# Performance work log

Hardware: AMD Instinct MI355X
Metric: run time of the kernel (lower is better)

Reference implementation:

```python
import jax, jax.numpy as jnp
import numpy as np

N_EMBD = 1024
N_HEAD = 16
HEAD_DIM = N_EMBD // N_HEAD


def setup_inputs() -> dict:
    key = jax.random.key(0)
    k1, k2, k3, k4, k5 = jax.random.split(key, 5)
    scale = 1.0 / np.sqrt(N_EMBD)
    x = jax.random.normal(k1, (4, 2048, N_EMBD), dtype=jnp.float32)
    W_qkv = jax.random.normal(k2, (N_EMBD, 3 * N_EMBD), dtype=jnp.float32) * scale
    b_qkv = jax.random.normal(k3, (3 * N_EMBD,), dtype=jnp.float32) * 0.01
    W_proj = jax.random.normal(k4, (N_EMBD, N_EMBD), dtype=jnp.float32) * scale
    b_proj = jax.random.normal(k5, (N_EMBD,), dtype=jnp.float32) * 0.01
    return {"x": x, "W_qkv": W_qkv, "b_qkv": b_qkv, "W_proj": W_proj, "b_proj": b_proj}


def reference(x, W_qkv, b_qkv, W_proj, b_proj):
    B, T, C = x.shape
    qkv = x @ W_qkv + b_qkv                      # [B,T,3C]
    q, k, v = jnp.split(qkv, 3, axis=-1)
    # [B,T,C] -> [B,H,T,D]
    def to_heads(t):
        return t.reshape(B, T, N_HEAD, HEAD_DIM).transpose(0, 2, 1, 3)
    q, k, v = to_heads(q), to_heads(k), to_heads(v)
    att = jnp.einsum('bhqd,bhkd->bhqk', q, k) / np.sqrt(HEAD_DIM)
    causal = jnp.tril(jnp.ones((T, T), dtype=bool))
    att = jnp.where(causal, att, -jnp.inf)
    att = jax.nn.softmax(att, axis=-1)
    y = jnp.einsum('bhqk,bhkd->bhqd', att, v)    # [B,H,T,D]
    y = y.transpose(0, 2, 1, 3).reshape(B, T, C)
    return y @ W_proj + b_proj
```

## Files before the change

### kernel.cpp

```cpp
#include <hip/hip_runtime.h>
#include <hip/hip_bf16.h>
#include <cstdint>

#define B_   4
#define T_   2048
#define C_   1024
#define H_   16
#define D_   64
#define TC3  3072
#define M_   (B_ * T_)

typedef short  bf16x8 __attribute__((ext_vector_type(8)));
typedef short  bf16x4 __attribute__((ext_vector_type(4)));
typedef float  f32x4  __attribute__((ext_vector_type(4)));

#define AS1(p) ((const __attribute__((address_space(1))) void*)(p))
#define AS3(p) ((__attribute__((address_space(3))) void*)(p))

__device__ inline float bf2f(unsigned short u) {
    union { unsigned int i; float f; } x; x.i = ((unsigned int)u) << 16; return x.f;
}
__device__ inline unsigned short f2bf(float f) {
    union { float f; unsigned int i; } x; x.f = f;
    return (unsigned short)((x.i + 0x7fffu + ((x.i >> 16) & 1u)) >> 16);
}
__device__ inline unsigned int cvtpk_bf16(float a, float b) {
    unsigned int r;
    asm("v_cvt_pk_bf16_f32 %0, %1, %2" : "=v"(r) : "v"(a), "v"(b));
    return r;
}
__device__ inline f32x4 mfma16x16x16(bf16x4 a, bf16x4 b, f32x4 c) {
#if __has_builtin(__builtin_amdgcn_mfma_f32_16x16x16bf16_1k)
    return __builtin_amdgcn_mfma_f32_16x16x16bf16_1k(a, b, c, 0, 0, 0);
#else
    asm("v_mfma_f32_16x16x16_bf16 %0, %1, %2, %0" : "+v"(c) : "v"(a), "v"(b));
    return c;
#endif
}

__global__ void cast_f32_bf16(const float* __restrict__ in,
                              unsigned short* __restrict__ out) {
    const size_t i = ((size_t)blockIdx.x * blockDim.x + threadIdx.x) * 8;
    f32x4 a = *(const f32x4*)(in + i);
    f32x4 b = *(const f32x4*)(in + i + 4);
    bf16x8 o;
#pragma unroll
    for (int j = 0; j < 4; ++j) { o[j] = (short)f2bf(a[j]); o[4 + j] = (short)f2bf(b[j]); }
    *(bf16x8*)(out + i) = o;
}

__global__ void transpose_cast(const float* __restrict__ in,
                               unsigned short* __restrict__ out, int R, int C) {
    __shared__ unsigned short tile[32][33];
    const int bc = blockIdx.x * 32, br = blockIdx.y * 32;
    const int tx = threadIdx.x & 31, ty = threadIdx.x >> 5;
#pragma unroll
    for (int i = 0; i < 4; ++i) {
        int r = ty + i * 8;
        tile[r][tx] = f2bf(in[(size_t)(br + r) * C + bc + tx]);
    }
    __syncthreads();
#pragma unroll
    for (int i = 0; i < 4; ++i) {
        int r = ty + i * 8;
        out[(size_t)(bc + r) * R + br + tx] = tile[tx][r];
    }
}

template <bool OUTF32>
__global__ __launch_bounds__(256, 2) void gemm_bt_bias(
    const unsigned short* __restrict__ A, const unsigned short* __restrict__ Bt,
    const float* __restrict__ bias, void* __restrict__ Cout,
    int M, int N, int K) {
    __shared__ unsigned short As[128 * 64];
    __shared__ unsigned short Bs[128 * 64];
    const int tid = threadIdx.x;
    const int wave = tid >> 6, lane = tid & 63;
    const int m0 = blockIdx.x * 128, n0 = blockIdx.y * 128;
    const int wr = (wave >> 1) * 64, wc = (wave & 1) * 64;

    f32x4 acc[4][4] = {};

    const int srow = (lane >> 3);
    const int scol = (lane & 7) * 8;

    for (int k0 = 0; k0 < K; k0 += 64) {
#pragma unroll
        for (int j = 0; j < 4; ++j) {
            const int chunk = wave * 4 + j;
            const int row = chunk * 8 + srow;
            __builtin_amdgcn_global_load_lds(
                AS1(A + (size_t)(m0 + row) * K + k0 + scol),
                AS3(As + chunk * 512), 16, 0, 0);
            __builtin_amdgcn_global_load_lds(
                AS1(Bt + (size_t)(n0 + row) * K + k0 + scol),
                AS3(Bs + chunk * 512), 16, 0, 0);
        }
        __syncthreads();
#pragma unroll
        for (int ph = 0; ph < 2; ++ph) {
            bf16x8 a[4], b[4];
#pragma unroll
            for (int i = 0; i < 4; ++i)
                a[i] = *(const bf16x8*)&As[(wr + i * 16 + (lane & 15)) * 64 + ph * 32 + (lane >> 4) * 8];
#pragma unroll
            for (int i = 0; i < 4; ++i)
                b[i] = *(const bf16x8*)&Bs[(wc + i * 16 + (lane & 15)) * 64 + ph * 32 + (lane >> 4) * 8];
            __builtin_amdgcn_s_setprio(1);
#pragma unroll
            for (int i = 0; i < 4; ++i)
#pragma unroll
                for (int j = 0; j < 4; ++j)
                    acc[i][j] = __builtin_amdgcn_mfma_f32_16x16x32_bf16(a[i], b[j], acc[i][j], 0, 0, 0);
            __builtin_amdgcn_s_setprio(0);
        }
        __syncthreads();
    }

#pragma unroll
    for (int i = 0; i < 4; ++i) {
        const int rowb = m0 + wr + i * 16 + (lane >> 4) * 4;
#pragma unroll
        for (int j = 0; j < 4; ++j) {
            const int col = n0 + wc + j * 16 + (lane & 15);
            const float bv = bias[col];
#pragma unroll
            for (int r = 0; r < 4; ++r) {
                const float v = acc[i][j][r] + bv;
                if (OUTF32)
                    ((float*)Cout)[(size_t)(rowb + r) * N + col] = v;
                else
                    ((unsigned short*)Cout)[(size_t)(rowb + r) * N + col] = f2bf(v);
            }
        }
    }
}

__global__ __launch_bounds__(512, 4) void attn_kernel(
    const unsigned short* __restrict__ QKV, unsigned short* __restrict__ Y) {
    __shared__ unsigned short Kl[64][72];
    __shared__ unsigned short Vt[64][72];

    const int tid = threadIdx.x, wave = tid >> 6, lane = tid & 63;
    const int bh = blockIdx.x;
    const int tq = 15 - (int)blockIdx.y;
    const int b = bh >> 4, h = bh & 15;
    const size_t rowbase = (size_t)b * T_ * TC3;
    const int l15 = lane & 15, lhi = lane >> 4;
    const int srow = tid >> 3;
    const int sseg = tid & 7;

    const int q0 = tq * 128 + wave * 16;
    const int ntiles = 2 * tq + 2;
    const int qv = q0 + l15;

    bf16x8 qf[2];
    {
        const unsigned short* p =
            QKV + rowbase + (size_t)(q0 + l15) * TC3 + h * 64 + lhi * 8;
        qf[0] = *(const bf16x8*)p;
        qf[1] = *(const bf16x8*)(p + 32);
#pragma unroll
        for (int hf = 0; hf < 2; ++hf)
#pragma unroll
            for (int j = 0; j < 8; ++j)
                qf[hf][j] = (short)f2bf(bf2f((unsigned short)qf[hf][j]) * 0.18033688011f);
    }

    float m2 = -1e30f, l_run = 0.f;
    f32x4 o[4] = {};

    {
        const unsigned short* src =
            QKV + rowbase + (size_t)srow * TC3 + C_ + h * 64 + sseg * 8;
        bf16x8 k8 = *(const bf16x8*)src;
        bf16x8 v8 = *(const bf16x8*)(src + C_);
        *(bf16x8*)&Kl[srow][sseg * 8] = k8;
        const int swz = srow ^ (sseg << 3);
#pragma unroll
        for (int j = 0; j < 8; ++j)
            Vt[sseg * 8 + j][swz] = (unsigned short)v8[j];
    }

    for (int t = 0; t < ntiles; ++t) {
        const int kv0 = t * 64;
        __syncthreads();

        bf16x8 pk8, pv8;
        const bool pf_valid = (t + 1 < ntiles);
        if (pf_valid) {
            const unsigned short* src =
                QKV + rowbase + (size_t)(kv0 + 64 + srow) * TC3 + C_ + h * 64 + sseg * 8;
            pk8 = *(const bf16x8*)src;
            pv8 = *(const bf16x8*)(src + C_);
        }

        if (q0 + 15 >= kv0) {
            f32x4 s[4];
            __builtin_amdgcn_s_setprio(1);
#pragma unroll
            for (int kt = 0; kt < 4; ++kt) {
                bf16x8 kf0 = *(const bf16x8*)&Kl[kt * 16 + l15][lhi * 8];
                bf16x8 kf1 = *(const bf16x8*)&Kl[kt * 16 + l15][32 + lhi * 8];
                f32x4 acc = {};
                acc = __builtin_amdgcn_mfma_f32_16x16x32_bf16(kf0, qf[0], acc, 0, 0, 0);
                acc = __builtin_amdgcn_mfma_f32_16x16x32_bf16(kf1, qf[1], acc, 0, 0, 0);
                s[kt] = acc;
            }
            __builtin_amdgcn_s_setprio(0);

            const bool needmask = (kv0 + 63 > q0);
            if (needmask) {
#pragma unroll
                for (int kt = 0; kt < 4; ++kt) {
                    const int kb = kv0 + kt * 16 + lhi * 4;
#pragma unroll
                    for (int r = 0; r < 4; ++r)
                        s[kt][r] = (kb + r <= qv) ? s[kt][r] : -1e30f;
                }
            }
            f32x4 vm;
#pragma unroll
            for (int r = 0; r < 4; ++r)
                vm[r] = fmaxf(fmaxf(s[0][r], s[1][r]), fmaxf(s[2][r], s[3][r]));
            float tmax = fmaxf(fmaxf(vm[0], vm[1]), fmaxf(vm[2], vm[3]));
            tmax = fmaxf(tmax, __shfl_xor(tmax, 16, 64));
            tmax = fmaxf(tmax, __shfl_xor(tmax, 32, 64));

            if (__any(tmax > m2 + 11.5416f)) {
                const float mnew = fmaxf(m2, tmax);
                const float corr = exp2f(m2 - mnew);
                m2 = mnew; l_run *= corr;
                float cq[4];
#pragma unroll
                for (int r = 0; r < 4; ++r)
                    cq[r] = __shfl(corr, lhi * 16 + lhi * 4 + r, 64);
#pragma unroll
                for (int dt = 0; dt < 4; ++dt)
#pragma unroll
                    for (int r = 0; r < 4; ++r) o[dt][r] *= cq[r];
            }
#pragma unroll
            for (int kt = 0; kt < 4; ++kt)
#pragma unroll
                for (int r = 0; r < 4; ++r)
                    s[kt][r] = exp2f(s[kt][r] - m2);
            {
                f32x4 vs;
#pragma unroll
                for (int r = 0; r < 4; ++r)
                    vs[r] = (s[0][r] + s[1][r]) + (s[2][r] + s[3][r]);
                float tsum = (vs[0] + vs[1]) + (vs[2] + vs[3]);
                tsum += __shfl_xor(tsum, 16, 64);
                tsum += __shfl_xor(tsum, 32, 64);
                l_run += tsum;
            }
            bf16x4 pa[4];
#pragma unroll
            for (int kt = 0; kt < 4; ++kt) {
                unsigned int pw[2];
                pw[0] = cvtpk_bf16(s[kt][0], s[kt][1]);
                pw[1] = cvtpk_bf16(s[kt][2], s[kt][3]);
                pa[kt] = *(const bf16x4*)pw;
            }

            __builtin_amdgcn_s_setprio(1);
#pragma unroll
            for (int dt = 0; dt < 4; ++dt) {
                const int d = dt * 16 + l15;
                const int xs = (d >> 3) << 3;
#pragma unroll
                for (int kt = 0; kt < 4; ++kt) {
                    bf16x4 vb = *(const bf16x4*)&Vt[d][(kt * 16 + lhi * 4) ^ xs];
                    o[dt] = mfma16x16x16(pa[kt], vb, o[dt]);
                }
            }
            __builtin_amdgcn_s_setprio(0);
        }

        __syncthreads();
        if (pf_valid) {
            *(bf16x8*)&Kl[srow][sseg * 8] = pk8;
            const int swz = srow ^ (sseg << 3);
#pragma unroll
            for (int j = 0; j < 8; ++j)
                Vt[sseg * 8 + j][swz] = (unsigned short)pv8[j];
        }
    }

    float rq[4];
#pragma unroll
    for (int r = 0; r < 4; ++r) {
        const float lq = __shfl(l_run, lhi * 16 + lhi * 4 + r, 64);
        rq[r] = 1.0f / lq;
    }
#pragma unroll
    for (int dt = 0; dt < 4; ++dt)
#pragma unroll
        for (int r = 0; r < 4; ++r) {
            const int q = q0 + lhi * 4 + r;
            const int d = dt * 16 + l15;
            Y[((size_t)b * T_ + q) * C_ + h * 64 + d] = f2bf(o[dt][r] * rq[r]);
        }
}

extern "C" void kernel_launch(void* const* d_in, const int* in_sizes, int n_in,
                              void* d_out, int out_size, void* d_ws, size_t ws_size,
                              hipStream_t stream) {
    const float* x     = (const float*)d_in[0];
    const float* Wqkv  = (const float*)d_in[1];
    const float* bqkv  = (const float*)d_in[2];
    const float* Wproj = (const float*)d_in[3];
    const float* bproj = (const float*)d_in[4];
    float* out = (float*)d_out;

    char* ws = (char*)d_ws;
    unsigned short* qkv    = (unsigned short*)(ws);
    unsigned short* yat    = (unsigned short*)(ws + 50331648);
    unsigned short* WqkvT  = (unsigned short*)(ws + 67108864);
    unsigned short* WprojT = (unsigned short*)(ws + 73400320);
    unsigned short* xb     = (unsigned short*)(ws + 75497472);

    cast_f32_bf16<<<dim3((M_ * C_) / (256 * 8)), dim3(256), 0, stream>>>(x, xb);
    transpose_cast<<<dim3(TC3 / 32, C_ / 32), dim3(256), 0, stream>>>(Wqkv, WqkvT, C_, TC3);
    transpose_cast<<<dim3(C_ / 32, C_ / 32), dim3(256), 0, stream>>>(Wproj, WprojT, C_, C_);
    gemm_bt_bias<false><<<dim3(M_ / 128, TC3 / 128), dim3(256), 0, stream>>>(xb, WqkvT, bqkv, qkv, M_, TC3, C_);
    attn_kernel<<<dim3(B_ * H_, 16), dim3(512), 0, stream>>>(qkv, yat);
    gemm_bt_bias<true><<<dim3(M_ / 128, C_ / 128), dim3(256), 0, stream>>>(yat, WprojT, bproj, out, M_, C_, C_);
}
```

Measured before the change: 186.9 us.

## Add 256x256 double-buffered QKV GEMM and pair causal attention tiles per block

```diff
diff --git a/kernel.cpp b/kernel.cpp
--- a/kernel.cpp
+++ b/kernel.cpp
@@ -67,10 +67,115 @@
     }
 }
 
-template <bool OUTF32>
+__global__ __launch_bounds__(512, 2) void gemm8_qkv(
+    const unsigned short* __restrict__ A, const unsigned short* __restrict__ Bt,
+    const float* __restrict__ bias, unsigned short* __restrict__ Cout,
+    int M, int N, int K) {
+    __shared__ unsigned short As[2 * 8192];
+    __shared__ unsigned short Bs[2 * 8192];
+
+    const int tid = threadIdx.x;
+    const int wave = tid >> 6, lane = tid & 63;
+    const int l15 = lane & 15, lhi = lane >> 4;
+    const int m0 = blockIdx.x * 256, n0 = blockIdx.y * 256;
+    const int wr = (wave >> 2) * 128;
+    const int wc = (wave & 3) * 64;
+
+    const int srow_s = tid >> 2;
+    const int scol_s = ((tid & 3) * 8) ^ ((srow_s & 3) << 3);
+    const int ldsw = (tid >> 6) * 512;
+
+    const int xcol = (lhi * 8) ^ ((l15 & 3) << 3);
+
+    f32x4 acc[8][4] = {};
+
+    {
+#pragma unroll
+        for (int g = 0; g < 2; ++g) {
+            __builtin_amdgcn_global_load_lds(
+                AS1(A + (size_t)(m0 + g * 128 + srow_s) * K + scol_s),
+                AS3(As + g * 4096 + ldsw), 16, 0, 0);
+            __builtin_amdgcn_global_load_lds(
+                AS1(Bt + (size_t)(n0 + g * 128 + srow_s) * K + scol_s),
+                AS3(Bs + g * 4096 + ldsw), 16, 0, 0);
+        }
+    }
+    __syncthreads();
+
+    for (int t = 0; t < 32; ++t) {
+        const int k0n = t * 32 + 32;
+        const int cur = t & 1, nxt = cur ^ 1;
+        const unsigned short* Ac = As + cur * 8192;
+        const unsigned short* Bc = Bs + cur * 8192;
+        unsigned short* An = As + nxt * 8192;
+        unsigned short* Bn = Bs + nxt * 8192;
+        const bool pf = (t < 31);
+
+        bf16x8 a[4], b[4];
+#pragma unroll
+        for (int i = 0; i < 4; ++i)
+            a[i] = *(const bf16x8*)&Ac[(wr + i * 16 + l15) * 32 + xcol];
+#pragma unroll
+        for (int j = 0; j < 4; ++j)
+            b[j] = *(const bf16x8*)&Bc[(wc + j * 16 + l15) * 32 + xcol];
+        if (pf) {
+            __builtin_amdgcn_global_load_lds(
+                AS1(A + (size_t)(m0 + srow_s) * K + k0n + scol_s),
+                AS3(An + ldsw), 16, 0, 0);
+            __builtin_amdgcn_global_load_lds(
+                AS1(Bt + (size_t)(n0 + srow_s) * K + k0n + scol_s),
+                AS3(Bn + ldsw), 16, 0, 0);
+        }
+        __builtin_amdgcn_s_barrier();
+        __builtin_amdgcn_s_setprio(1);
+#pragma unroll
+        for (int i = 0; i < 4; ++i)
+#pragma unroll
+            for (int j = 0; j < 4; ++j)
+                acc[i][j] = __builtin_amdgcn_mfma_f32_16x16x32_bf16(a[i], b[j], acc[i][j], 0, 0, 0);
+        __builtin_amdgcn_s_setprio(0);
+        __builtin_amdgcn_s_barrier();
+
+        bf16x8 a2[4];
+#pragma unroll
+        for (int i = 0; i < 4; ++i)
+            a2[i] = *(const bf16x8*)&Ac[(wr + (i + 4) * 16 + l15) * 32 + xcol];
+        if (pf) {
+            __builtin_amdgcn_global_load_lds(
+                AS1(A + (size_t)(m0 + 128 + srow_s) * K + k0n + scol_s),
+                AS3(An + 4096 + ldsw), 16, 0, 0);
+            __builtin_amdgcn_global_load_lds(
+                AS1(Bt + (size_t)(n0 + 128 + srow_s) * K + k0n + scol_s),
+                AS3(Bn + 4096 + ldsw), 16, 0, 0);
+        }
+        __builtin_amdgcn_s_barrier();
+        __builtin_amdgcn_s_setprio(1);
+#pragma unroll
+        for (int i = 0; i < 4; ++i)
+#pragma unroll
+            for (int j = 0; j < 4; ++j)
+                acc[i + 4][j] = __builtin_amdgcn_mfma_f32_16x16x32_bf16(a2[i], b[j], acc[i + 4][j], 0, 0, 0);
+        __builtin_amdgcn_s_setprio(0);
+        __syncthreads();
+    }
+
+#pragma unroll
+    for (int i = 0; i < 8; ++i) {
+        const int rowb = m0 + wr + i * 16 + lhi * 4;
+#pragma unroll
+        for (int j = 0; j < 4; ++j) {
+            const int col = n0 + wc + j * 16 + l15;
+            const float bv = bias[col];
+#pragma unroll
+            for (int r = 0; r < 4; ++r)
+                Cout[(size_t)(rowb + r) * N + col] = f2bf(acc[i][j][r] + bv);
+        }
+    }
+}
+
 __global__ __launch_bounds__(256, 2) void gemm_bt_bias(
     const unsigned short* __restrict__ A, const unsigned short* __restrict__ Bt,
-    const float* __restrict__ bias, void* __restrict__ Cout,
+    const float* __restrict__ bias, float* __restrict__ Cout,
     int M, int N, int K) {
     __shared__ unsigned short As[128 * 64];
     __shared__ unsigned short Bs[128 * 64];
@@ -125,13 +230,8 @@
             const int col = n0 + wc + j * 16 + (lane & 15);
             const float bv = bias[col];
 #pragma unroll
-            for (int r = 0; r < 4; ++r) {
-                const float v = acc[i][j][r] + bv;
-                if (OUTF32)
-                    ((float*)Cout)[(size_t)(rowb + r) * N + col] = v;
-                else
-                    ((unsigned short*)Cout)[(size_t)(rowb + r) * N + col] = f2bf(v);
-            }
+            for (int r = 0; r < 4; ++r)
+                Cout[(size_t)(rowb + r) * N + col] = acc[i][j][r] + bv;
         }
     }
 }
@@ -143,165 +243,170 @@
 
     const int tid = threadIdx.x, wave = tid >> 6, lane = tid & 63;
     const int bh = blockIdx.x;
-    const int tq = 15 - (int)blockIdx.y;
+    const int pr = blockIdx.y;
     const int b = bh >> 4, h = bh & 15;
     const size_t rowbase = (size_t)b * T_ * TC3;
     const int l15 = lane & 15, lhi = lane >> 4;
     const int srow = tid >> 3;
     const int sseg = tid & 7;
 
-    const int q0 = tq * 128 + wave * 16;
-    const int ntiles = 2 * tq + 2;
-    const int qv = q0 + l15;
-
-    bf16x8 qf[2];
-    {
-        const unsigned short* p =
-            QKV + rowbase + (size_t)(q0 + l15) * TC3 + h * 64 + lhi * 8;
-        qf[0] = *(const bf16x8*)p;
-        qf[1] = *(const bf16x8*)(p + 32);
-#pragma unroll
-        for (int hf = 0; hf < 2; ++hf)
+    for (int sp = 0; sp < 2; ++sp) {
+        const int tq = sp ? (15 - pr) : pr;
+        const int qb = tq * 128;
+        const int q0 = qb + wave * 16;
+        const int ntiles = 2 * tq + 2;
+        const int qv = q0 + l15;
+
+        bf16x8 qf[2];
+        {
+            const unsigned short* p =
+                QKV + rowbase + (size_t)(q0 + l15) * TC3 + h * 64 + lhi * 8;
+            qf[0] = *(const bf16x8*)p;
+            qf[1] = *(const bf16x8*)(p + 32);
+#pragma unroll
+            for (int hf = 0; hf < 2; ++hf)
+#pragma unroll
+                for (int j = 0; j < 8; ++j)
+                    qf[hf][j] = (short)f2bf(bf2f((unsigned short)qf[hf][j]) * 0.18033688011f);
+        }
+
+        float m2 = -1e30f, l_run = 0.f;
+        f32x4 o[4] = {};
+
+        __syncthreads();
+        {
+            const unsigned short* src =
+                QKV + rowbase + (size_t)srow * TC3 + C_ + h * 64 + sseg * 8;
+            bf16x8 k8 = *(const bf16x8*)src;
+            bf16x8 v8 = *(const bf16x8*)(src + C_);
+            *(bf16x8*)&Kl[srow][sseg * 8] = k8;
+            const int swz = srow ^ (sseg << 3);
 #pragma unroll
             for (int j = 0; j < 8; ++j)
-                qf[hf][j] = (short)f2bf(bf2f((unsigned short)qf[hf][j]) * 0.18033688011f);
-    }
-
-    float m2 = -1e30f, l_run = 0.f;
-    f32x4 o[4] = {};
-
-    {
-        const unsigned short* src =
-            QKV + rowbase + (size_t)srow * TC3 + C_ + h * 64 + sseg * 8;
-        bf16x8 k8 = *(const bf16x8*)src;
-        bf16x8 v8 = *(const bf16x8*)(src + C_);
-        *(bf16x8*)&Kl[srow][sseg * 8] = k8;
-        const int swz = srow ^ (sseg << 3);
-#pragma unroll
-        for (int j = 0; j < 8; ++j)
-            Vt[sseg * 8 + j][swz] = (unsigned short)v8[j];
-    }
-
-    for (int t = 0; t < ntiles; ++t) {
-        const int kv0 = t * 64;
-        __syncthreads();
-
-        bf16x8 pk8, pv8;
-        const bool pf_valid = (t + 1 < ntiles);
-        if (pf_valid) {
-            const unsigned short* src =
-                QKV + rowbase + (size_t)(kv0 + 64 + srow) * TC3 + C_ + h * 64 + sseg * 8;
-            pk8 = *(const bf16x8*)src;
-            pv8 = *(const bf16x8*)(src + C_);
-        }
-
-        if (q0 + 15 >= kv0) {
-            f32x4 s[4];
-            __builtin_amdgcn_s_setprio(1);
-#pragma unroll
-            for (int kt = 0; kt < 4; ++kt) {
-                bf16x8 kf0 = *(const bf16x8*)&Kl[kt * 16 + l15][lhi * 8];
-                bf16x8 kf1 = *(const bf16x8*)&Kl[kt * 16 + l15][32 + lhi * 8];
-                f32x4 acc = {};
-                acc = __builtin_amdgcn_mfma_f32_16x16x32_bf16(kf0, qf[0], acc, 0, 0, 0);
-                acc = __builtin_amdgcn_mfma_f32_16x16x32_bf16(kf1, qf[1], acc, 0, 0, 0);
-                s[kt] = acc;
+                Vt[sseg * 8 + j][swz] = (unsigned short)v8[j];
+        }
+
+        for (int t = 0; t < ntiles; ++t) {
+            const int kv0 = t * 64;
+            __syncthreads();
+
+            bf16x8 pk8, pv8;
+            const bool pf_valid = (t + 1 < ntiles);
+            if (pf_valid) {
+                const unsigned short* src =
+                    QKV + rowbase + (size_t)(kv0 + 64 + srow) * TC3 + C_ + h * 64 + sseg * 8;
+                pk8 = *(const bf16x8*)src;
+                pv8 = *(const bf16x8*)(src + C_);
             }
-            __builtin_amdgcn_s_setprio(0);
-
-            const bool needmask = (kv0 + 63 > q0);
-            if (needmask) {
+
+            if (q0 + 15 >= kv0) {
+                f32x4 s[4];
+                __builtin_amdgcn_s_setprio(1);
 #pragma unroll
                 for (int kt = 0; kt < 4; ++kt) {
-                    const int kb = kv0 + kt * 16 + lhi * 4;
+                    bf16x8 kf0 = *(const bf16x8*)&Kl[kt * 16 + l15][lhi * 8];
+                    bf16x8 kf1 = *(const bf16x8*)&Kl[kt * 16 + l15][32 + lhi * 8];
+                    f32x4 acc = {};
+                    acc = __builtin_amdgcn_mfma_f32_16x16x32_bf16(kf0, qf[0], acc, 0, 0, 0);
+                    acc = __builtin_amdgcn_mfma_f32_16x16x32_bf16(kf1, qf[1], acc, 0, 0, 0);
+                    s[kt] = acc;
+                }
+                __builtin_amdgcn_s_setprio(0);
+
+                const bool needmask = (kv0 + 63 > q0);
+                if (needmask) {
+#pragma unroll
+                    for (int kt = 0; kt < 4; ++kt) {
+                        const int kb = kv0 + kt * 16 + lhi * 4;
+#pragma unroll
+                        for (int r = 0; r < 4; ++r)
+                            s[kt][r] = (kb + r <= qv) ? s[kt][r] : -1e30f;
+                    }
+                }
+                f32x4 vm;
+#pragma unroll
+                for (int r = 0; r < 4; ++r)
+                    vm[r] = fmaxf(fmaxf(s[0][r], s[1][r]), fmaxf(s[2][r], s[3][r]));
+                float tmax = fmaxf(fmaxf(vm[0], vm[1]), fmaxf(vm[2], vm[3]));
+                tmax = fmaxf(tmax, __shfl_xor(tmax, 16, 64));
+                tmax = fmaxf(tmax, __shfl_xor(tmax, 32, 64));
+
+                if (__any(tmax > m2 + 11.5416f)) {
+                    const float mnew = fmaxf(m2, tmax);
+                    const float corr = exp2f(m2 - mnew);
+                    m2 = mnew; l_run *= corr;
+                    float cq[4];
 #pragma unroll
                     for (int r = 0; r < 4; ++r)
-                        s[kt][r] = (kb + r <= qv) ? s[kt][r] : -1e30f;
-                }
+                        cq[r] = __shfl(corr, lhi * 16 + lhi * 4 + r, 64);
+#pragma unroll
+                    for (int dt = 0; dt < 4; ++dt)
+#pragma unroll
+                        for (int r = 0; r < 4; ++r) o[dt][r] *= cq[r];
+                }
+#pragma unroll
+                for (int kt = 0; kt < 4; ++kt)
+#pragma unroll
+                    for (int r = 0; r < 4; ++r)
+                        s[kt][r] = exp2f(s[kt][r] - m2);
+                {
+                    f32x4 vs;
+#pragma unroll
+                    for (int r = 0; r < 4; ++r)
+                        vs[r] = (s[0][r] + s[1][r]) + (s[2][r] + s[3][r]);
+                    float tsum = (vs[0] + vs[1]) + (vs[2] + vs[3]);
+                    tsum += __shfl_xor(tsum, 16, 64);
+                    tsum += __shfl_xor(tsum, 32, 64);
+                    l_run += tsum;
+                }
+                bf16x4 pa[4];
+#pragma unroll
+                for (int kt = 0; kt < 4; ++kt) {
+                    unsigned int pw[2];
+                    pw[0] = cvtpk_bf16(s[kt][0], s[kt][1]);
+                    pw[1] = cvtpk_bf16(s[kt][2], s[kt][3]);
+                    pa[kt] = *(const bf16x4*)pw;
+                }
+
+                __builtin_amdgcn_s_setprio(1);
+#pragma unroll
+                for (int dt = 0; dt < 4; ++dt) {
+                    const int d = dt * 16 + l15;
+                    const int xs = (d >> 3) << 3;
+#pragma unroll
+                    for (int kt = 0; kt < 4; ++kt) {
+                        bf16x4 vb = *(const bf16x4*)&Vt[d][(kt * 16 + lhi * 4) ^ xs];
+                        o[dt] = mfma16x16x16(pa[kt], vb, o[dt]);
+                    }
+                }
+                __builtin_amdgcn_s_setprio(0);
             }
-            f32x4 vm;
-#pragma unroll
-            for (int r = 0; r < 4; ++r)
-                vm[r] = fmaxf(fmaxf(s[0][r], s[1][r]), fmaxf(s[2][r], s[3][r]));
-            float tmax = fmaxf(fmaxf(vm[0], vm[1]), fmaxf(vm[2], vm[3]));
-            tmax = fmaxf(tmax, __shfl_xor(tmax, 16, 64));
-            tmax = fmaxf(tmax, __shfl_xor(tmax, 32, 64));
-
-            if (__any(tmax > m2 + 11.5416f)) {
-                const float mnew = fmaxf(m2, tmax);
-                const float corr = exp2f(m2 - mnew);
-                m2 = mnew; l_run *= corr;
-                float cq[4];
-#pragma unroll
-                for (int r = 0; r < 4; ++r)
-                    cq[r] = __shfl(corr, lhi * 16 + lhi * 4 + r, 64);
-#pragma unroll
-                for (int dt = 0; dt < 4; ++dt)
-#pragma unroll
-                    for (int r = 0; r < 4; ++r) o[dt][r] *= cq[r];
+
+            __syncthreads();
+            if (pf_valid) {
+                *(bf16x8*)&Kl[srow][sseg * 8] = pk8;
+                const int swz = srow ^ (sseg << 3);
+#pragma unroll
+                for (int j = 0; j < 8; ++j)
+                    Vt[sseg * 8 + j][swz] = (unsigned short)pv8[j];
             }
-#pragma unroll
-            for (int kt = 0; kt < 4; ++kt)
-#pragma unroll
-                for (int r = 0; r < 4; ++r)
-                    s[kt][r] = exp2f(s[kt][r] - m2);
-            {
-                f32x4 vs;
-#pragma unroll
-                for (int r = 0; r < 4; ++r)
-                    vs[r] = (s[0][r] + s[1][r]) + (s[2][r] + s[3][r]);
-                float tsum = (vs[0] + vs[1]) + (vs[2] + vs[3]);
-                tsum += __shfl_xor(tsum, 16, 64);
-                tsum += __shfl_xor(tsum, 32, 64);
-                l_run += tsum;
+        }
+
+        float rq[4];
+#pragma unroll
+        for (int r = 0; r < 4; ++r) {
+            const float lq = __shfl(l_run, lhi * 16 + lhi * 4 + r, 64);
+            rq[r] = 1.0f / lq;
+        }
+#pragma unroll
+        for (int dt = 0; dt < 4; ++dt)
+#pragma unroll
+            for (int r = 0; r < 4; ++r) {
+                const int q = q0 + lhi * 4 + r;
+                const int d = dt * 16 + l15;
+                Y[((size_t)b * T_ + q) * C_ + h * 64 + d] = f2bf(o[dt][r] * rq[r]);
             }
-            bf16x4 pa[4];
-#pragma unroll
-            for (int kt = 0; kt < 4; ++kt) {
-                unsigned int pw[2];
-                pw[0] = cvtpk_bf16(s[kt][0], s[kt][1]);
-                pw[1] = cvtpk_bf16(s[kt][2], s[kt][3]);
-                pa[kt] = *(const bf16x4*)pw;
-            }
-
-            __builtin_amdgcn_s_setprio(1);
-#pragma unroll
-            for (int dt = 0; dt < 4; ++dt) {
-                const int d = dt * 16 + l15;
-                const int xs = (d >> 3) << 3;
-#pragma unroll
-                for (int kt = 0; kt < 4; ++kt) {
-                    bf16x4 vb = *(const bf16x4*)&Vt[d][(kt * 16 + lhi * 4) ^ xs];
-                    o[dt] = mfma16x16x16(pa[kt], vb, o[dt]);
-                }
-            }
-            __builtin_amdgcn_s_setprio(0);
-        }
-
-        __syncthreads();
-        if (pf_valid) {
-            *(bf16x8*)&Kl[srow][sseg * 8] = pk8;
-            const int swz = srow ^ (sseg << 3);
-#pragma unroll
-            for (int j = 0; j < 8; ++j)
-                Vt[sseg * 8 + j][swz] = (unsigned short)pv8[j];
-        }
-    }
-
-    float rq[4];
-#pragma unroll
-    for (int r = 0; r < 4; ++r) {
-        const float lq = __shfl(l_run, lhi * 16 + lhi * 4 + r, 64);
-        rq[r] = 1.0f / lq;
-    }
-#pragma unroll
-    for (int dt = 0; dt < 4; ++dt)
-#pragma unroll
-        for (int r = 0; r < 4; ++r) {
-            const int q = q0 + lhi * 4 + r;
-            const int d = dt * 16 + l15;
-            Y[((size_t)b * T_ + q) * C_ + h * 64 + d] = f2bf(o[dt][r] * rq[r]);
-        }
+    }
 }
 
 extern "C" void kernel_launch(void* const* d_in, const int* in_sizes, int n_in,
@@ -324,7 +429,7 @@
     cast_f32_bf16<<<dim3((M_ * C_) / (256 * 8)), dim3(256), 0, stream>>>(x, xb);
     transpose_cast<<<dim3(TC3 / 32, C_ / 32), dim3(256), 0, stream>>>(Wqkv, WqkvT, C_, TC3);
     transpose_cast<<<dim3(C_ / 32, C_ / 32), dim3(256), 0, stream>>>(Wproj, WprojT, C_, C_);
-    gemm_bt_bias<false><<<dim3(M_ / 128, TC3 / 128), dim3(256), 0, stream>>>(xb, WqkvT, bqkv, qkv, M_, TC3, C_);
-    attn_kernel<<<dim3(B_ * H_, 16), dim3(512), 0, stream>>>(qkv, yat);
-    gemm_bt_bias<true><<<dim3(M_ / 128, C_ / 128), dim3(256), 0, stream>>>(yat, WprojT, bproj, out, M_, C_, C_);
-}
+    gemm8_qkv<<<dim3(M_ / 256, TC3 / 256), dim3(512), 0, stream>>>(xb, WqkvT, bqkv, qkv, M_, TC3, C_);
+    attn_kernel<<<dim3(B_ * H_, 8), dim3(512), 0, stream>>>(qkv, yat);
+    gemm_bt_bias<<<dim3(M_ / 128, C_ / 128), dim3(256), 0, stream>>>(yat, WprojT, bproj, out, M_, C_, C_);
+}
```

New measurement: 195.2 us. +4.5%, slower.

## Double-buffer GEMM LDS tiles and pair causal attention query blocks per workgroup

Applied to the files above, without the earlier changes.

```diff
diff --git a/kernel.cpp b/kernel.cpp
--- a/kernel.cpp
+++ b/kernel.cpp
@@ -72,8 +72,8 @@
     const unsigned short* __restrict__ A, const unsigned short* __restrict__ Bt,
     const float* __restrict__ bias, void* __restrict__ Cout,
     int M, int N, int K) {
-    __shared__ unsigned short As[128 * 64];
-    __shared__ unsigned short Bs[128 * 64];
+    __shared__ unsigned short As[2][128 * 64];
+    __shared__ unsigned short Bs[2][128 * 64];
     const int tid = threadIdx.x;
     const int wave = tid >> 6, lane = tid & 63;
     const int m0 = blockIdx.x * 128, n0 = blockIdx.y * 128;
@@ -84,28 +84,45 @@
     const int srow = (lane >> 3);
     const int scol = (lane & 7) * 8;
 
-    for (int k0 = 0; k0 < K; k0 += 64) {
-#pragma unroll
-        for (int j = 0; j < 4; ++j) {
-            const int chunk = wave * 4 + j;
-            const int row = chunk * 8 + srow;
-            __builtin_amdgcn_global_load_lds(
-                AS1(A + (size_t)(m0 + row) * K + k0 + scol),
-                AS3(As + chunk * 512), 16, 0, 0);
-            __builtin_amdgcn_global_load_lds(
-                AS1(Bt + (size_t)(n0 + row) * K + k0 + scol),
-                AS3(Bs + chunk * 512), 16, 0, 0);
-        }
-        __syncthreads();
+#pragma unroll
+    for (int j = 0; j < 4; ++j) {
+        const int chunk = wave * 4 + j;
+        const int row = chunk * 8 + srow;
+        __builtin_amdgcn_global_load_lds(
+            AS1(A + (size_t)(m0 + row) * K + scol),
+            AS3(&As[0][chunk * 512]), 16, 0, 0);
+        __builtin_amdgcn_global_load_lds(
+            AS1(Bt + (size_t)(n0 + row) * K + scol),
+            AS3(&Bs[0][chunk * 512]), 16, 0, 0);
+    }
+    __syncthreads();
+
+    const int NT = K >> 6;
+    for (int t = 0; t < NT; ++t) {
+        const int cur = t & 1, nxt = cur ^ 1;
+        if (t + 1 < NT) {
+            const int k0n = (t + 1) << 6;
+#pragma unroll
+            for (int j = 0; j < 4; ++j) {
+                const int chunk = wave * 4 + j;
+                const int row = chunk * 8 + srow;
+                __builtin_amdgcn_global_load_lds(
+                    AS1(A + (size_t)(m0 + row) * K + k0n + scol),
+                    AS3(&As[nxt][chunk * 512]), 16, 0, 0);
+                __builtin_amdgcn_global_load_lds(
+                    AS1(Bt + (size_t)(n0 + row) * K + k0n + scol),
+                    AS3(&Bs[nxt][chunk * 512]), 16, 0, 0);
+            }
+        }
 #pragma unroll
         for (int ph = 0; ph < 2; ++ph) {
             bf16x8 a[4], b[4];
 #pragma unroll
             for (int i = 0; i < 4; ++i)
-                a[i] = *(const bf16x8*)&As[(wr + i * 16 + (lane & 15)) * 64 + ph * 32 + (lane >> 4) * 8];
+                a[i] = *(const bf16x8*)&As[cur][(wr + i * 16 + (lane & 15)) * 64 + ph * 32 + (lane >> 4) * 8];
 #pragma unroll
             for (int i = 0; i < 4; ++i)
-                b[i] = *(const bf16x8*)&Bs[(wc + i * 16 + (lane & 15)) * 64 + ph * 32 + (lane >> 4) * 8];
+                b[i] = *(const bf16x8*)&Bs[cur][(wc + i * 16 + (lane & 15)) * 64 + ph * 32 + (lane >> 4) * 8];
             __builtin_amdgcn_s_setprio(1);
 #pragma unroll
             for (int i = 0; i < 4; ++i)
@@ -143,165 +160,170 @@
 
     const int tid = threadIdx.x, wave = tid >> 6, lane = tid & 63;
     const int bh = blockIdx.x;
-    const int tq = 15 - (int)blockIdx.y;
+    const int pr = blockIdx.y;
     const int b = bh >> 4, h = bh & 15;
     const size_t rowbase = (size_t)b * T_ * TC3;
     const int l15 = lane & 15, lhi = lane >> 4;
     const int srow = tid >> 3;
     const int sseg = tid & 7;
 
-    const int q0 = tq * 128 + wave * 16;
-    const int ntiles = 2 * tq + 2;
-    const int qv = q0 + l15;
-
-    bf16x8 qf[2];
-    {
-        const unsigned short* p =
-            QKV + rowbase + (size_t)(q0 + l15) * TC3 + h * 64 + lhi * 8;
-        qf[0] = *(const bf16x8*)p;
-        qf[1] = *(const bf16x8*)(p + 32);
-#pragma unroll
-        for (int hf = 0; hf < 2; ++hf)
+    for (int sp = 0; sp < 2; ++sp) {
+        const int tq = sp ? (15 - pr) : pr;
+        const int qb = tq * 128;
+        const int q0 = qb + wave * 16;
+        const int ntiles = 2 * tq + 2;
+        const int qv = q0 + l15;
+
+        bf16x8 qf[2];
+        {
+            const unsigned short* p =
+                QKV + rowbase + (size_t)(q0 + l15) * TC3 + h * 64 + lhi * 8;
+            qf[0] = *(const bf16x8*)p;
+            qf[1] = *(const bf16x8*)(p + 32);
+#pragma unroll
+            for (int hf = 0; hf < 2; ++hf)
+#pragma unroll
+                for (int j = 0; j < 8; ++j)
+                    qf[hf][j] = (short)f2bf(bf2f((unsigned short)qf[hf][j]) * 0.18033688011f);
+        }
+
+        float m2 = -1e30f, l_run = 0.f;
+        f32x4 o[4] = {};
+
+        __syncthreads();
+        {
+            const unsigned short* src =
+                QKV + rowbase + (size_t)srow * TC3 + C_ + h * 64 + sseg * 8;
+            bf16x8 k8 = *(const bf16x8*)src;
+            bf16x8 v8 = *(const bf16x8*)(src + C_);
+            *(bf16x8*)&Kl[srow][sseg * 8] = k8;
+            const int swz = srow ^ (sseg << 3);
 #pragma unroll
             for (int j = 0; j < 8; ++j)
-                qf[hf][j] = (short)f2bf(bf2f((unsigned short)qf[hf][j]) * 0.18033688011f);
-    }
-
-    float m2 = -1e30f, l_run = 0.f;
-    f32x4 o[4] = {};
-
-    {
-        const unsigned short* src =
-            QKV + rowbase + (size_t)srow * TC3 + C_ + h * 64 + sseg * 8;
-        bf16x8 k8 = *(const bf16x8*)src;
-        bf16x8 v8 = *(const bf16x8*)(src + C_);
-        *(bf16x8*)&Kl[srow][sseg * 8] = k8;
-        const int swz = srow ^ (sseg << 3);
-#pragma unroll
-        for (int j = 0; j < 8; ++j)
-            Vt[sseg * 8 + j][swz] = (unsigned short)v8[j];
-    }
-
-    for (int t = 0; t < ntiles; ++t) {
-        const int kv0 = t * 64;
-        __syncthreads();
-
-        bf16x8 pk8, pv8;
-        const bool pf_valid = (t + 1 < ntiles);
-        if (pf_valid) {
-            const unsigned short* src =
-                QKV + rowbase + (size_t)(kv0 + 64 + srow) * TC3 + C_ + h * 64 + sseg * 8;
-            pk8 = *(const bf16x8*)src;
-            pv8 = *(const bf16x8*)(src + C_);
-        }
-
-        if (q0 + 15 >= kv0) {
-            f32x4 s[4];
-            __builtin_amdgcn_s_setprio(1);
-#pragma unroll
-            for (int kt = 0; kt < 4; ++kt) {
-                bf16x8 kf0 = *(const bf16x8*)&Kl[kt * 16 + l15][lhi * 8];
-                bf16x8 kf1 = *(const bf16x8*)&Kl[kt * 16 + l15][32 + lhi * 8];
-                f32x4 acc = {};
-                acc = __builtin_amdgcn_mfma_f32_16x16x32_bf16(kf0, qf[0], acc, 0, 0, 0);
-                acc = __builtin_amdgcn_mfma_f32_16x16x32_bf16(kf1, qf[1], acc, 0, 0, 0);
-                s[kt] = acc;
-            }
-            __builtin_amdgcn_s_setprio(0);
-
-            const bool needmask = (kv0 + 63 > q0);
-            if (needmask) {
+                Vt[sseg * 8 + j][swz] = (unsigned short)v8[j];
+        }
+
+        for (int t = 0; t < ntiles; ++t) {
+            const int kv0 = t * 64;
+            __syncthreads();
+
+            bf16x8 pk8, pv8;
+            const bool pf_valid = (t + 1 < ntiles);
+            if (pf_valid) {
+                const unsigned short* src =
+                    QKV + rowbase + (size_t)(kv0 + 64 + srow) * TC3 + C_ + h * 64 + sseg * 8;
+                pk8 = *(const bf16x8*)src;
+                pv8 = *(const bf16x8*)(src + C_);
+            }
+
+            if (q0 + 15 >= kv0) {
+                f32x4 s[4];
+                __builtin_amdgcn_s_setprio(1);
 #pragma unroll
                 for (int kt = 0; kt < 4; ++kt) {
-                    const int kb = kv0 + kt * 16 + lhi * 4;
+                    bf16x8 kf0 = *(const bf16x8*)&Kl[kt * 16 + l15][lhi * 8];
+                    bf16x8 kf1 = *(const bf16x8*)&Kl[kt * 16 + l15][32 + lhi * 8];
+                    f32x4 acc = {};
+                    acc = __builtin_amdgcn_mfma_f32_16x16x32_bf16(kf0, qf[0], acc, 0, 0, 0);
+                    acc = __builtin_amdgcn_mfma_f32_16x16x32_bf16(kf1, qf[1], acc, 0, 0, 0);
+                    s[kt] = acc;
+                }
+                __builtin_amdgcn_s_setprio(0);
+
+                const bool needmask = (kv0 + 63 > q0);
+                if (needmask) {
+#pragma unroll
+                    for (int kt = 0; kt < 4; ++kt) {
+                        const int kb = kv0 + kt * 16 + lhi * 4;
+#pragma unroll
+                        for (int r = 0; r < 4; ++r)
+                            s[kt][r] = (kb + r <= qv) ? s[kt][r] : -1e30f;
+                    }
+                }
+                f32x4 vm;
+#pragma unroll
+                for (int r = 0; r < 4; ++r)
+                    vm[r] = fmaxf(fmaxf(s[0][r], s[1][r]), fmaxf(s[2][r], s[3][r]));
+                float tmax = fmaxf(fmaxf(vm[0], vm[1]), fmaxf(vm[2], vm[3]));
+                tmax = fmaxf(tmax, __shfl_xor(tmax, 16, 64));
+                tmax = fmaxf(tmax, __shfl_xor(tmax, 32, 64));
+
+                if (__any(tmax > m2 + 11.5416f)) {
+                    const float mnew = fmaxf(m2, tmax);
+                    const float corr = exp2f(m2 - mnew);
+                    m2 = mnew; l_run *= corr;
+                    float cq[4];
 #pragma unroll
                     for (int r = 0; r < 4; ++r)
-                        s[kt][r] = (kb + r <= qv) ? s[kt][r] : -1e30f;
-                }
-            }
-            f32x4 vm;
-#pragma unroll
-            for (int r = 0; r < 4; ++r)
-                vm[r] = fmaxf(fmaxf(s[0][r], s[1][r]), fmaxf(s[2][r], s[3][r]));
-            float tmax = fmaxf(fmaxf(vm[0], vm[1]), fmaxf(vm[2], vm[3]));
-            tmax = fmaxf(tmax, __shfl_xor(tmax, 16, 64));
-            tmax = fmaxf(tmax, __shfl_xor(tmax, 32, 64));
-
-            if (__any(tmax > m2 + 11.5416f)) {
-                const float mnew = fmaxf(m2, tmax);
-                const float corr = exp2f(m2 - mnew);
-                m2 = mnew; l_run *= corr;
-                float cq[4];
-#pragma unroll
-                for (int r = 0; r < 4; ++r)
-                    cq[r] = __shfl(corr, lhi * 16 + lhi * 4 + r, 64);
-#pragma unroll
-                for (int dt = 0; dt < 4; ++dt)
-#pragma unroll
-                    for (int r = 0; r < 4; ++r) o[dt][r] *= cq[r];
-            }
-#pragma unroll
-            for (int kt = 0; kt < 4; ++kt)
-#pragma unroll
-                for (int r = 0; r < 4; ++r)
-                    s[kt][r] = exp2f(s[kt][r] - m2);
-            {
-                f32x4 vs;
-#pragma unroll
-                for (int r = 0; r < 4; ++r)
-                    vs[r] = (s[0][r] + s[1][r]) + (s[2][r] + s[3][r]);
-                float tsum = (vs[0] + vs[1]) + (vs[2] + vs[3]);
-                tsum += __shfl_xor(tsum, 16, 64);
-                tsum += __shfl_xor(tsum, 32, 64);
-                l_run += tsum;
-            }
-            bf16x4 pa[4];
-#pragma unroll
-            for (int kt = 0; kt < 4; ++kt) {
-                unsigned int pw[2];
-                pw[0] = cvtpk_bf16(s[kt][0], s[kt][1]);
-                pw[1] = cvtpk_bf16(s[kt][2], s[kt][3]);
-                pa[kt] = *(const bf16x4*)pw;
-            }
-
-            __builtin_amdgcn_s_setprio(1);
-#pragma unroll
-            for (int dt = 0; dt < 4; ++dt) {
+                        cq[r] = __shfl(corr, lhi * 16 + lhi * 4 + r, 64);
+#pragma unroll
+                    for (int dt = 0; dt < 4; ++dt)
+#pragma unroll
+                        for (int r = 0; r < 4; ++r) o[dt][r] *= cq[r];
+                }
+#pragma unroll
+                for (int kt = 0; kt < 4; ++kt)
+#pragma unroll
+                    for (int r = 0; r < 4; ++r)
+                        s[kt][r] = exp2f(s[kt][r] - m2);
+                {
+                    f32x4 vs;
+#pragma unroll
+                    for (int r = 0; r < 4; ++r)
+                        vs[r] = (s[0][r] + s[1][r]) + (s[2][r] + s[3][r]);
+                    float tsum = (vs[0] + vs[1]) + (vs[2] + vs[3]);
+                    tsum += __shfl_xor(tsum, 16, 64);
+                    tsum += __shfl_xor(tsum, 32, 64);
+                    l_run += tsum;
+                }
+                bf16x4 pa[4];
+#pragma unroll
+                for (int kt = 0; kt < 4; ++kt) {
+                    unsigned int pw[2];
+                    pw[0] = cvtpk_bf16(s[kt][0], s[kt][1]);
+                    pw[1] = cvtpk_bf16(s[kt][2], s[kt][3]);
+                    pa[kt] = *(const bf16x4*)pw;
+                }
+
+                __builtin_amdgcn_s_setprio(1);
+#pragma unroll
+                for (int dt = 0; dt < 4; ++dt) {
+                    const int d = dt * 16 + l15;
+                    const int xs = (d >> 3) << 3;
+#pragma unroll
+                    for (int kt = 0; kt < 4; ++kt) {
+                        bf16x4 vb = *(const bf16x4*)&Vt[d][(kt * 16 + lhi * 4) ^ xs];
+                        o[dt] = mfma16x16x16(pa[kt], vb, o[dt]);
+                    }
+                }
+                __builtin_amdgcn_s_setprio(0);
+            }
+
+            __syncthreads();
+            if (pf_valid) {
+                *(bf16x8*)&Kl[srow][sseg * 8] = pk8;
+                const int swz = srow ^ (sseg << 3);
+#pragma unroll
+                for (int j = 0; j < 8; ++j)
+                    Vt[sseg * 8 + j][swz] = (unsigned short)pv8[j];
+            }
+        }
+
+        float rq[4];
+#pragma unroll
+        for (int r = 0; r < 4; ++r) {
+            const float lq = __shfl(l_run, lhi * 16 + lhi * 4 + r, 64);
+            rq[r] = 1.0f / lq;
+        }
+#pragma unroll
+        for (int dt = 0; dt < 4; ++dt)
+#pragma unroll
+            for (int r = 0; r < 4; ++r) {
+                const int q = q0 + lhi * 4 + r;
                 const int d = dt * 16 + l15;
-                const int xs = (d >> 3) << 3;
-#pragma unroll
-                for (int kt = 0; kt < 4; ++kt) {
-                    bf16x4 vb = *(const bf16x4*)&Vt[d][(kt * 16 + lhi * 4) ^ xs];
-                    o[dt] = mfma16x16x16(pa[kt], vb, o[dt]);
-                }
-            }
-            __builtin_amdgcn_s_setprio(0);
-        }
-
-        __syncthreads();
-        if (pf_valid) {
-            *(bf16x8*)&Kl[srow][sseg * 8] = pk8;
-            const int swz = srow ^ (sseg << 3);
-#pragma unroll
-            for (int j = 0; j < 8; ++j)
-                Vt[sseg * 8 + j][swz] = (unsigned short)pv8[j];
-        }
-    }
-
-    float rq[4];
-#pragma unroll
-    for (int r = 0; r < 4; ++r) {
-        const float lq = __shfl(l_run, lhi * 16 + lhi * 4 + r, 64);
-        rq[r] = 1.0f / lq;
-    }
-#pragma unroll
-    for (int dt = 0; dt < 4; ++dt)
-#pragma unroll
-        for (int r = 0; r < 4; ++r) {
-            const int q = q0 + lhi * 4 + r;
-            const int d = dt * 16 + l15;
-            Y[((size_t)b * T_ + q) * C_ + h * 64 + d] = f2bf(o[dt][r] * rq[r]);
-        }
+                Y[((size_t)b * T_ + q) * C_ + h * 64 + d] = f2bf(o[dt][r] * rq[r]);
+            }
+    }
 }
 
 extern "C" void kernel_launch(void* const* d_in, const int* in_sizes, int n_in,
@@ -325,6 +347,6 @@
     transpose_cast<<<dim3(TC3 / 32, C_ / 32), dim3(256), 0, stream>>>(Wqkv, WqkvT, C_, TC3);
     transpose_cast<<<dim3(C_ / 32, C_ / 32), dim3(256), 0, stream>>>(Wproj, WprojT, C_, C_);
     gemm_bt_bias<false><<<dim3(M_ / 128, TC3 / 128), dim3(256), 0, stream>>>(xb, WqkvT, bqkv, qkv, M_, TC3, C_);
-    attn_kernel<<<dim3(B_ * H_, 16), dim3(512), 0, stream>>>(qkv, yat);
+    attn_kernel<<<dim3(B_ * H_, 8), dim3(512), 0, stream>>>(qkv, yat);
     gemm_bt_bias<true><<<dim3(M_ / 128, C_ / 128), dim3(256), 0, stream>>>(yat, WprojT, bproj, out, M_, C_, C_);
 }
```

Result: slower. 194.6 us (+4.1%).
